# Kernel optimization log

Hardware: AMD Instinct MI355X
Metric: run time of the kernel (lower is better)

The kernel has to match this reference:

```python
import jax, jax.numpy as jnp
import numpy as np

D_MODEL = 512
N_HEADS = 8
D_HEAD = D_MODEL // N_HEADS
SCALE = D_HEAD ** -0.5


def _rel_shift(x):
    # x: (b, h, qlen, klen) -> Transformer-XL relative shift
    b, h, qlen, klen = x.shape
    x = jnp.pad(x, ((0, 0), (0, 0), (0, 0), (1, 0)))        # (b,h,q,k+1)
    x = x.reshape(b, h, klen + 1, qlen)
    x = x[:, :, 1:, :].reshape(b, h, qlen, klen)
    return x


def setup_inputs() -> dict:
    key = jax.random.key(0)
    ks = jax.random.split(key, 12)
    B, S = 2, 2048
    P = 2 * S - 1
    w = lambda k, shape: (jax.random.normal(k, shape, jnp.float32) * 0.02)
    return {
        "x": jax.random.normal(ks[0], (B, S, D_MODEL), jnp.float32),
        "pos_emb": jax.random.normal(ks[1], (P, D_MODEL), jnp.float32),
        "Wq": w(ks[2], (D_MODEL, D_MODEL)), "bq": jnp.zeros((D_MODEL,), jnp.float32),
        "Wk": w(ks[3], (D_MODEL, D_MODEL)), "bk": jnp.zeros((D_MODEL,), jnp.float32),
        "Wv": w(ks[4], (D_MODEL, D_MODEL)), "bv": jnp.zeros((D_MODEL,), jnp.float32),
        "Wp": w(ks[5], (D_MODEL, D_MODEL)),
        "Wo": w(ks[6], (D_MODEL, D_MODEL)), "bo": jnp.zeros((D_MODEL,), jnp.float32),
        "pos_bias_u": w(ks[7], (N_HEADS, D_HEAD)),
        "pos_bias_v": w(ks[8], (N_HEADS, D_HEAD)),
    }


def reference(x, pos_emb, Wq, bq, Wk, bk, Wv, bv, Wp, Wo, bo, pos_bias_u, pos_bias_v):
    B, S, _ = x.shape
    # projections (torch Linear: y = x @ W^T + b; here W stored as (in, out))
    q = (x @ Wq + bq).reshape(B, S, N_HEADS, D_HEAD)
    k = (x @ Wk + bk).reshape(B, S, N_HEADS, D_HEAD)
    v = (x @ Wv + bv).reshape(B, S, N_HEADS, D_HEAD)
    p = (pos_emb @ Wp).reshape(-1, N_HEADS, D_HEAD)  # (2S-1, H, D)

    # content score: (q + u) @ k^T  -> (B,H,S,S)
    content = jnp.einsum("bshd,bthd->bhst", q + pos_bias_u, k)
    # position score: (q + v_bias) @ p^T -> (B,H,S,2S-1), then rel_shift
    pos = jnp.einsum("bshd,phd->bhsp", q + pos_bias_v, p)
    pos = _rel_shift(pos)[..., :S]  # trim to kv_len

    attn = jax.nn.softmax((content + pos) * SCALE, axis=-1)
    out = jnp.einsum("bhst,bthd->bshd", attn, v).reshape(B, S, D_MODEL)
    out = out @ Wo + bo
    return out
```

## Files before the change

kernel.cpp:

```cpp
#include <hip/hip_runtime.h>

#define DM    512
#define NH    8
#define DH    64
#define SEQ   2048
#define PLEN  4095
#define NB    2
#define ATT_SCALE 0.125f

typedef __attribute__((ext_vector_type(8))) _Float16 half8;
typedef __attribute__((ext_vector_type(4))) float   floatx4;

__device__ __forceinline__ void gll16(const _Float16* g, _Float16* l) {
    __builtin_amdgcn_global_load_lds(
        (const __attribute__((address_space(1))) void*)g,
        (__attribute__((address_space(3))) void*)l, 16, 0, 0);
}

__global__ __launch_bounds__(256)
void prep(const float* __restrict__ x, const float* __restrict__ pe,
          const float* __restrict__ W0, const float* __restrict__ W1,
          const float* __restrict__ W2, const float* __restrict__ W3,
          const float* __restrict__ W4,
          _Float16* __restrict__ x16, _Float16* __restrict__ pe16,
          _Float16* __restrict__ Wt)
{
    __shared__ _Float16 tile[64 * 72];
    const int z = blockIdx.z;
    const int t = threadIdx.x;

    if (z < 2) {
        const float* src = z ? pe : x;
        _Float16* dst = z ? pe16 : x16;
        const long n = z ? (long)PLEN * DM : (long)NB * SEQ * DM;
        const long i = ((long)blockIdx.x * 256 + t) * 8;
        if (i >= n) return;
        float4 f0 = *(const float4*)(src + i);
        float4 f1 = *(const float4*)(src + i + 4);
        half8 o;
        o[0] = (_Float16)f0.x; o[1] = (_Float16)f0.y;
        o[2] = (_Float16)f0.z; o[3] = (_Float16)f0.w;
        o[4] = (_Float16)f1.x; o[5] = (_Float16)f1.y;
        o[6] = (_Float16)f1.z; o[7] = (_Float16)f1.w;
        *(half8*)(dst + i) = o;
        return;
    }
    if (blockIdx.x >= 64) return;
    const int wz = z - 2;
    const float* W = (wz == 0) ? W0 : (wz == 1) ? W1 : (wz == 2) ? W2
                   : (wz == 3) ? W3 : W4;
    _Float16* dst_base = Wt + (size_t)wz * DM * DM;
    const int n0 = (blockIdx.x & 7) * 64, k0 = (blockIdx.x >> 3) * 64;
    {
        const int kr = t >> 2, nch = (t & 3) * 16;
        const float* src = W + (size_t)(k0 + kr) * DM + n0 + nch;
        float4 f0 = *(const float4*)(src + 0);
        float4 f1 = *(const float4*)(src + 4);
        float4 f2 = *(const float4*)(src + 8);
        float4 f3 = *(const float4*)(src + 12);
        _Float16* trow = &tile[kr * 72 + nch];
        trow[0]  = (_Float16)f0.x; trow[1]  = (_Float16)f0.y;
        trow[2]  = (_Float16)f0.z; trow[3]  = (_Float16)f0.w;
        trow[4]  = (_Float16)f1.x; trow[5]  = (_Float16)f1.y;
        trow[6]  = (_Float16)f1.z; trow[7]  = (_Float16)f1.w;
        trow[8]  = (_Float16)f2.x; trow[9]  = (_Float16)f2.y;
        trow[10] = (_Float16)f2.z; trow[11] = (_Float16)f2.w;
        trow[12] = (_Float16)f3.x; trow[13] = (_Float16)f3.y;
        trow[14] = (_Float16)f3.z; trow[15] = (_Float16)f3.w;
    }
    __syncthreads();
    {
        const int nr = t >> 2, kch = (t & 3) * 16;
        half8 o0, o1;
#pragma unroll
        for (int i = 0; i < 8; ++i) o0[i] = tile[(kch + i) * 72 + nr];
#pragma unroll
        for (int i = 0; i < 8; ++i) o1[i] = tile[(kch + 8 + i) * 72 + nr];
        _Float16* dst = dst_base + (size_t)(n0 + nr) * DM + k0 + kch;
        *(half8*)dst = o0;
        *(half8*)(dst + 8) = o1;
    }
}

__global__ __launch_bounds__(256)
void gemm_qkvp(const _Float16* __restrict__ X, const _Float16* __restrict__ Pe,
               const _Float16* __restrict__ Wt,
               const float* __restrict__ bq, const float* __restrict__ bk,
               const float* __restrict__ bv, const float* __restrict__ bu,
               const float* __restrict__ bvb,
               _Float16* __restrict__ qu16, _Float16* __restrict__ qv16,
               _Float16* __restrict__ k16, _Float16* __restrict__ vt16,
               _Float16* __restrict__ p16)
{
    __shared__ _Float16 aS[64 * 72];
    __shared__ _Float16 wS[64 * 72];

    const int t = threadIdx.x;
    const int w = t >> 6, lane = t & 63, quad = lane >> 4, l16 = lane & 15;
    const int z = blockIdx.z;
    const int n0 = blockIdx.x * 64;
    const int m0 = blockIdx.y * 64;
    const int srow = t >> 2, sch = (t & 3) * 16;
    const _Float16* A = (z == 3) ? Pe : X;
    const _Float16* Wz = Wt + (size_t)z * DM * DM;

    int arow = m0 + srow;
    if (z == 3 && arow > PLEN - 1) arow = PLEN - 1;
    const _Float16* arowp = A + (size_t)arow * DM + sch;
    const _Float16* wrowp = Wz + (size_t)(n0 + srow) * DM + sch;

    floatx4 acc[4];
#pragma unroll
    for (int ct = 0; ct < 4; ++ct) acc[ct] = (floatx4){0.f, 0.f, 0.f, 0.f};

    half8 pa0 = *(const half8*)arowp;
    half8 pa1 = *(const half8*)(arowp + 8);
    half8 pw0 = *(const half8*)wrowp;
    half8 pw1 = *(const half8*)(wrowp + 8);

    for (int k0 = 0; k0 < DM; k0 += 64) {
        __syncthreads();
        *(half8*)&aS[srow * 72 + sch]     = pa0;
        *(half8*)&aS[srow * 72 + sch + 8] = pa1;
        *(half8*)&wS[srow * 72 + sch]     = pw0;
        *(half8*)&wS[srow * 72 + sch + 8] = pw1;
        __syncthreads();
        if (k0 + 64 < DM) {
            pa0 = *(const half8*)(arowp + k0 + 64);
            pa1 = *(const half8*)(arowp + k0 + 72);
            pw0 = *(const half8*)(wrowp + k0 + 64);
            pw1 = *(const half8*)(wrowp + k0 + 72);
        }
#pragma unroll
        for (int kb = 0; kb < 2; ++kb) {
            half8 af = *(const half8*)&aS[(16 * w + l16) * 72 + kb * 32 + quad * 8];
#pragma unroll
            for (int ct = 0; ct < 4; ++ct) {
                half8 bf = *(const half8*)&wS[(16 * ct + l16) * 72 + kb * 32 + quad * 8];
                acc[ct] = __builtin_amdgcn_mfma_f32_16x16x32_f16(af, bf, acc[ct], 0, 0, 0);
            }
        }
    }

    const int h = n0 >> 6;
    if (z == 0) {
#pragma unroll
        for (int ct = 0; ct < 4; ++ct) {
            const int n = n0 + 16 * ct + l16;
            const float bval = bq[n], uval = bu[n], vval = bvb[n];
#pragma unroll
            for (int r = 0; r < 4; ++r) {
                const int m = m0 + 16 * w + 4 * quad + r;
                const int b = m >> 11, s = m & 2047;
                const size_t dst = ((size_t)((h * NB + b) * SEQ) + s) * DH + (n & 63);
                const float q = acc[ct][r] + bval;
                qu16[dst] = (_Float16)((q + uval) * ATT_SCALE);
                qv16[dst] = (_Float16)((q + vval) * ATT_SCALE);
            }
        }
    } else if (z == 1) {
#pragma unroll
        for (int ct = 0; ct < 4; ++ct) {
            const int n = n0 + 16 * ct + l16;
            const float bval = bk[n];
#pragma unroll
            for (int r = 0; r < 4; ++r) {
                const int m = m0 + 16 * w + 4 * quad + r;
                const int b = m >> 11, s = m & 2047;
                k16[((size_t)((h * NB + b) * SEQ) + s) * DH + (n & 63)] =
                    (_Float16)(acc[ct][r] + bval);
            }
        }
    } else if (z == 2) {
        __syncthreads();
#pragma unroll
        for (int ct = 0; ct < 4; ++ct) {
            const float bval = bv[n0 + 16 * ct + l16];
#pragma unroll
            for (int r = 0; r < 4; ++r)
                aS[(16 * w + 4 * quad + r) * 72 + 16 * ct + l16] =
                    (_Float16)(acc[ct][r] + bval);
        }
        __syncthreads();
        const int b = m0 >> 11, s0 = m0 & 2047;
        const int drow = t >> 2;
        half8 o0, o1;
#pragma unroll
        for (int i = 0; i < 8; ++i) o0[i] = aS[(sch + i) * 72 + drow];
#pragma unroll
        for (int i = 0; i < 8; ++i) o1[i] = aS[(sch + 8 + i) * 72 + drow];
        _Float16* dst = vt16 + ((size_t)((h * NB + b) * DH) + drow) * SEQ + s0 + sch;
        *(half8*)dst = o0;
        *(half8*)(dst + 8) = o1;
    } else {
#pragma unroll
        for (int ct = 0; ct < 4; ++ct) {
            const int n = n0 + 16 * ct + l16;
#pragma unroll
            for (int r = 0; r < 4; ++r) {
                const int m = m0 + 16 * w + 4 * quad + r;
                if (m < PLEN)
                    p16[((size_t)h * PLEN + m) * DH + (n & 63)] = (_Float16)acc[ct][r];
            }
        }
    }
}

__global__ __launch_bounds__(256, 3)
void relattn_mfma(const _Float16* __restrict__ QU,
                  const _Float16* __restrict__ QV,
                  const _Float16* __restrict__ Kp,
                  const _Float16* __restrict__ VT,
                  const _Float16* __restrict__ Pp,
                  float* __restrict__ Opart,
                  float* __restrict__ Lpart)
{
    __shared__ _Float16 kbuf[2 * 4096];
    __shared__ _Float16 vbuf[4096];
    __shared__ _Float16 pring[2 * 4096];
    __shared__ _Float16 tS[64 * 72];

    const int t = threadIdx.x;
    const int w = t >> 6, lane = t & 63, quad = lane >> 4, l16 = lane & 15;
    const int i0 = blockIdx.x * 64;
    const int h = blockIdx.y;
    const int b = blockIdx.z & 1, jh = blockIdx.z >> 1;
    const size_t hb = (size_t)(h * NB + b);
    const int cbase = 48 - 16 * w;
    const int jbeg = jh * (SEQ / 2), jend = jbeg + (SEQ / 2);

    half8 qa[2], va[2];
    {
        const _Float16* qrow = QU + (hb * SEQ + i0 + 16 * w + l16) * DH + quad * 8;
        const _Float16* vrow = QV + (hb * SEQ + i0 + 16 * w + l16) * DH + quad * 8;
        qa[0] = *(const half8*)qrow;       qa[1] = *(const half8*)(qrow + 32);
        va[0] = *(const half8*)vrow;       va[1] = *(const half8*)(vrow + 32);
    }

    floatx4 O[4];
    float lsum[4] = {0.f, 0.f, 0.f, 0.f};
#pragma unroll
    for (int ct = 0; ct < 4; ++ct) O[ct] = (floatx4){0.f, 0.f, 0.f, 0.f};

    const _Float16* Kbase = Kp + hb * SEQ * DH;
    const _Float16* Vbase = VT + hb * DH * SEQ;
    const _Float16* Pbase = Pp + (size_t)h * PLEN * DH;
    const int rbase0 = (SEQ - 1) - i0 - 63;
    const int w0beg  = rbase0 + jbeg;

    const int kx = l16 & 7;
    const int hox0 = ((quad) ^ kx) * 8;
    const int hox1 = ((4 + quad) ^ kx) * 8;

    const int l3 = lane >> 3, pos = lane & 7;

    int prow64[5], pcar[5];
#pragma unroll
    for (int c2 = 0; c2 < 5; ++c2) {
        const int off = cbase + 16 * c2 + l16;
        prow64[c2] = (off & 63) * 64;
        pcar[c2]   = (off >> 6) & 1;
    }

#define STAGE_K(DST, J0)                                                       \
    { _Pragma("unroll") for (int I = 0; I < 2; ++I) {                          \
        const int cid = w * 2 + I;                                             \
        const int row = cid * 8 + l3;                                          \
        gll16(Kbase + (size_t)((J0) + row) * DH + ((pos ^ l3) << 3),           \
              (DST) + cid * 512); } }

#define STAGE_V(J0)                                                            \
    { _Pragma("unroll") for (int I = 0; I < 2; ++I) {                          \
        const int cid = w * 2 + I;                                             \
        const int row = cid * 8 + l3;                                          \
        gll16(Vbase + (size_t)row * SEQ + (J0) + ((pos ^ l3) << 3),            \
              vbuf + cid * 512); } }

#define STAGE_P(RELB)                                                         \
    { _Float16* pdst = pring + ((((RELB) >> 6) & 1) * 4096);                  \
      _Pragma("unroll") for (int I = 0; I < 2; ++I) {                         \
        const int cid = w * 2 + I;                                            \
        int ar = w0beg + (RELB) + cid * 8 + l3;                               \
        if (ar > PLEN - 1) ar = PLEN - 1;                                     \
        gll16(Pbase + (size_t)ar * DH + ((pos ^ l3) << 3),                    \
              pdst + cid * 512); } }

    STAGE_K(kbuf, jbeg);
    STAGE_P(0);
    STAGE_P(64);

    int cur = 0, par = 0;
    for (int j0 = jbeg; j0 < jend; j0 += 64) {
        asm volatile("s_waitcnt vmcnt(0)" ::: "memory");
        __builtin_amdgcn_s_barrier();
        asm volatile("" ::: "memory");

        const _Float16* kS = kbuf + cur * 4096;
        const bool more = (j0 + 64 < jend);

        STAGE_V(j0);
        if (more) STAGE_K(kbuf + (cur ^ 1) * 4096, j0 + 64);

        floatx4 Tacc[5];
#pragma unroll
        for (int c2 = 0; c2 < 5; ++c2) Tacc[c2] = (floatx4){0.f, 0.f, 0.f, 0.f};
#pragma unroll
        for (int c2 = 0; c2 < 5; ++c2) {
            const _Float16* pp = pring + ((pcar[c2] ^ par) * 4096) + prow64[c2];
            half8 bf0 = *(const half8*)(pp + hox0);
            half8 bf1 = *(const half8*)(pp + hox1);
            Tacc[c2] = __builtin_amdgcn_mfma_f32_16x16x32_f16(va[0], bf0, Tacc[c2], 0, 0, 0);
            Tacc[c2] = __builtin_amdgcn_mfma_f32_16x16x32_f16(va[1], bf1, Tacc[c2], 0, 0, 0);
        }

        asm volatile("" ::: "memory");
        __builtin_amdgcn_s_barrier();
        asm volatile("" ::: "memory");
        if (more) STAGE_P((j0 - jbeg) + 128);

        floatx4 Sc[4];
#pragma unroll
        for (int ct = 0; ct < 4; ++ct) Sc[ct] = (floatx4){0.f, 0.f, 0.f, 0.f};
#pragma unroll
        for (int ct = 0; ct < 4; ++ct) {
            half8 bf0 = *(const half8*)&kS[(16 * ct + l16) * 64 + hox0];
            half8 bf1 = *(const half8*)&kS[(16 * ct + l16) * 64 + hox1];
            Sc[ct] = __builtin_amdgcn_mfma_f32_16x16x32_f16(qa[0], bf0, Sc[ct], 0, 0, 0);
            Sc[ct] = __builtin_amdgcn_mfma_f32_16x16x32_f16(qa[1], bf1, Sc[ct], 0, 0, 0);
        }

#pragma unroll
        for (int r = 0; r < 4; ++r) {
            const int u  = l16 - 4 * quad - r + 15;
            const int dl = u & 15;
            const int s  = u >> 4;
            const int pidx = (((quad << 4) | dl) << 2);
            float rot[5];
#pragma unroll
            for (int c2 = 0; c2 < 5; ++c2)
                rot[c2] = __int_as_float(__builtin_amdgcn_ds_bpermute(
                    pidx, __float_as_int(Tacc[c2][r])));
#pragma unroll
            for (int ct = 0; ct < 4; ++ct) {
                const float tv = s ? rot[ct + 1] : rot[ct];
                const float e = __expf(Sc[ct][r] + tv);
                Sc[ct][r] = e;
                lsum[r] += e;
            }
        }

#pragma unroll
        for (int ct = 0; ct < 4; ++ct)
#pragma unroll
            for (int r = 0; r < 4; ++r)
                tS[(16 * w + 4 * quad + r) * 72 + 16 * ct + l16] = (_Float16)Sc[ct][r];
        asm volatile("" ::: "memory");

        if (more) asm volatile("s_waitcnt vmcnt(4)" ::: "memory");
        else      asm volatile("s_waitcnt vmcnt(0)" ::: "memory");
        __builtin_amdgcn_s_barrier();
        asm volatile("" ::: "memory");

#pragma unroll
        for (int kb = 0; kb < 2; ++kb) {
            half8 af = *(const half8*)&tS[(16 * w + l16) * 72 + kb * 32 + quad * 8];
            const int hox = kb ? hox1 : hox0;
#pragma unroll
            for (int ct = 0; ct < 4; ++ct) {
                half8 bf = *(const half8*)&vbuf[(16 * ct + l16) * 64 + hox];
                O[ct] = __builtin_amdgcn_mfma_f32_16x16x32_f16(af, bf, O[ct], 0, 0, 0);
            }
        }
        asm volatile("" ::: "memory");
        cur ^= 1; par ^= 1;
    }
#undef STAGE_K
#undef STAGE_V
#undef STAGE_P

    float* Op = Opart + (size_t)jh * NB * SEQ * DM;
    float* Lp = Lpart + (size_t)jh * NH * NB * SEQ;
#pragma unroll
    for (int r = 0; r < 4; ++r) {
#pragma unroll
        for (int m = 1; m < 16; m <<= 1) lsum[r] += __shfl_xor(lsum[r], m);
        const int row = i0 + 16 * w + 4 * quad + r;
        if (l16 == 0) Lp[hb * SEQ + row] = lsum[r];
        float* orow = Op + (size_t)(b * SEQ + row) * DM + h * DH;
#pragma unroll
        for (int ct = 0; ct < 4; ++ct)
            orow[16 * ct + l16] = O[ct][r];
    }
}

__global__ __launch_bounds__(256)
void attn_combine(const float* __restrict__ O0, const float* __restrict__ O1,
                  const float* __restrict__ L0, const float* __restrict__ L1,
                  _Float16* __restrict__ Out)
{
    const int e = (blockIdx.x * 256 + threadIdx.x) * 8;
    const int m = e >> 9;
    const int col = e & 511;
    const int h = col >> 6;
    const int b = m >> 11, i = m & 2047;
    const int li = (h * NB + b) * SEQ + i;
    const float inv = 1.f / (L0[li] + L1[li]);
    float4 a0 = *(const float4*)(O0 + e);
    float4 a1 = *(const float4*)(O0 + e + 4);
    float4 c0 = *(const float4*)(O1 + e);
    float4 c1 = *(const float4*)(O1 + e + 4);
    half8 o;
    o[0] = (_Float16)((a0.x + c0.x) * inv);
    o[1] = (_Float16)((a0.y + c0.y) * inv);
    o[2] = (_Float16)((a0.z + c0.z) * inv);
    o[3] = (_Float16)((a0.w + c0.w) * inv);
    o[4] = (_Float16)((a1.x + c1.x) * inv);
    o[5] = (_Float16)((a1.y + c1.y) * inv);
    o[6] = (_Float16)((a1.z + c1.z) * inv);
    o[7] = (_Float16)((a1.w + c1.w) * inv);
    *(half8*)(Out + e) = o;
}

__global__ __launch_bounds__(256)
void gemm_out(const _Float16* __restrict__ A, const _Float16* __restrict__ Wt,
              const float* __restrict__ bias, float* __restrict__ Out)
{
    __shared__ _Float16 aS[64 * 72];
    __shared__ _Float16 wS[64 * 72];

    const int t = threadIdx.x;
    const int w = t >> 6, lane = t & 63, quad = lane >> 4, l16 = lane & 15;
    const int n0 = blockIdx.x * 64;
    const int m0 = blockIdx.y * 64;
    const int srow = t >> 2, sch = (t & 3) * 16;

    const _Float16* arowp = A + (size_t)(m0 + srow) * DM + sch;
    const _Float16* wrowp = Wt + (size_t)(n0 + srow) * DM + sch;

    floatx4 acc[4];
#pragma unroll
    for (int ct = 0; ct < 4; ++ct) acc[ct] = (floatx4){0.f, 0.f, 0.f, 0.f};

    half8 pa0 = *(const half8*)arowp;
    half8 pa1 = *(const half8*)(arowp + 8);
    half8 pw0 = *(const half8*)wrowp;
    half8 pw1 = *(const half8*)(wrowp + 8);

    for (int k0 = 0; k0 < DM; k0 += 64) {
        __syncthreads();
        *(half8*)&aS[srow * 72 + sch]     = pa0;
        *(half8*)&aS[srow * 72 + sch + 8] = pa1;
        *(half8*)&wS[srow * 72 + sch]     = pw0;
        *(half8*)&wS[srow * 72 + sch + 8] = pw1;
        __syncthreads();
        if (k0 + 64 < DM) {
            pa0 = *(const half8*)(arowp + k0 + 64);
            pa1 = *(const half8*)(arowp + k0 + 72);
            pw0 = *(const half8*)(wrowp + k0 + 64);
            pw1 = *(const half8*)(wrowp + k0 + 72);
        }
#pragma unroll
        for (int kb = 0; kb < 2; ++kb) {
            half8 af = *(const half8*)&aS[(16 * w + l16) * 72 + kb * 32 + quad * 8];
#pragma unroll
            for (int ct = 0; ct < 4; ++ct) {
                half8 bf = *(const half8*)&wS[(16 * ct + l16) * 72 + kb * 32 + quad * 8];
                acc[ct] = __builtin_amdgcn_mfma_f32_16x16x32_f16(af, bf, acc[ct], 0, 0, 0);
            }
        }
    }

#pragma unroll
    for (int ct = 0; ct < 4; ++ct) {
        const int n = n0 + 16 * ct + l16;
        const float bval = bias[n];
#pragma unroll
        for (int r = 0; r < 4; ++r) {
            const int m = m0 + 16 * w + 4 * quad + r;
            Out[(size_t)m * DM + n] = acc[ct][r] + bval;
        }
    }
}

extern "C" void kernel_launch(void* const* d_in, const int* in_sizes, int n_in,
                              void* d_out, int out_size, void* d_ws, size_t ws_size,
                              hipStream_t stream)
{
    (void)in_sizes; (void)n_in; (void)out_size; (void)ws_size;
    const float* x   = (const float*)d_in[0];
    const float* pe  = (const float*)d_in[1];
    const float* Wq  = (const float*)d_in[2];
    const float* bq  = (const float*)d_in[3];
    const float* Wk  = (const float*)d_in[4];
    const float* bk  = (const float*)d_in[5];
    const float* Wv  = (const float*)d_in[6];
    const float* bv  = (const float*)d_in[7];
    const float* Wp  = (const float*)d_in[8];
    const float* Wo  = (const float*)d_in[9];
    const float* bo  = (const float*)d_in[10];
    const float* pbu = (const float*)d_in[11];
    const float* pbv = (const float*)d_in[12];
    float* out = (float*)d_out;

    const size_t nX  = (size_t)NB * SEQ * DM;
    const size_t nPe = (size_t)PLEN * DM;
    const size_t nW  = (size_t)DM * DM;
    const size_t nH  = (size_t)NH * NB * SEQ * DH;
    const size_t nPh = (size_t)NH * PLEN * DH;
    const size_t nL  = (size_t)NH * NB * SEQ;

    _Float16* x16  = (_Float16*)d_ws;
    _Float16* pe16 = x16 + nX;
    _Float16* wt   = pe16 + nPe;
    _Float16* qu16 = wt + 5 * nW;
    _Float16* qv16 = qu16 + nH;
    _Float16* k16  = qv16 + nH;
    _Float16* vt16 = k16 + nH;
    _Float16* p16  = vt16 + nH;
    _Float16* ow16 = p16 + nPh;
    float*    opart = (float*)(ow16 + nX);
    float*    lpart = opart + 2 * nX;

    dim3 blk(256);
    prep<<<dim3(1024, 1, 7), blk, 0, stream>>>(x, pe, Wq, Wk, Wv, Wp, Wo,
                                               x16, pe16, wt);
    gemm_qkvp<<<dim3(8, 64, 4), blk, 0, stream>>>(x16, pe16, wt,
                                                  bq, bk, bv, pbu, pbv,
                                                  qu16, qv16, k16, vt16, p16);
    relattn_mfma<<<dim3(SEQ / 64, NH, NB * 2), blk, 0, stream>>>(
        qu16, qv16, k16, vt16, p16, opart, lpart);
    attn_combine<<<dim3((unsigned)(nX / (256 * 8))), blk, 0, stream>>>(
        opart, opart + nX, lpart, lpart + nL, ow16);
    gemm_out<<<dim3(8, 64), blk, 0, stream>>>(ow16, wt + 4 * nW, bo, out);
}
```

Baseline: 187.5 us.

## Retile QKVP projection GEMM to 128x128 with async LDS double buffering

```diff
diff --git a/kernel.cpp b/kernel.cpp
--- a/kernel.cpp
+++ b/kernel.cpp
@@ -92,116 +92,149 @@
                _Float16* __restrict__ k16, _Float16* __restrict__ vt16,
                _Float16* __restrict__ p16)
 {
-    __shared__ _Float16 aS[64 * 72];
-    __shared__ _Float16 wS[64 * 72];
+    __shared__ _Float16 smem[32768];
 
     const int t = threadIdx.x;
     const int w = t >> 6, lane = t & 63, quad = lane >> 4, l16 = lane & 15;
+    const int wr = w >> 1, wc = w & 1;
+    const int l3 = lane >> 3, pos = lane & 7;
     const int z = blockIdx.z;
-    const int n0 = blockIdx.x * 64;
-    const int m0 = blockIdx.y * 64;
-    const int srow = t >> 2, sch = (t & 3) * 16;
+    const int n0 = blockIdx.x * 128;
+    const int m0 = blockIdx.y * 128;
+
     const _Float16* A = (z == 3) ? Pe : X;
     const _Float16* Wz = Wt + (size_t)z * DM * DM;
 
-    int arow = m0 + srow;
-    if (z == 3 && arow > PLEN - 1) arow = PLEN - 1;
-    const _Float16* arowp = A + (size_t)arow * DM + sch;
-    const _Float16* wrowp = Wz + (size_t)(n0 + srow) * DM + sch;
-
-    floatx4 acc[4];
-#pragma unroll
-    for (int ct = 0; ct < 4; ++ct) acc[ct] = (floatx4){0.f, 0.f, 0.f, 0.f};
-
-    half8 pa0 = *(const half8*)arowp;
-    half8 pa1 = *(const half8*)(arowp + 8);
-    half8 pw0 = *(const half8*)wrowp;
-    half8 pw1 = *(const half8*)(wrowp + 8);
-
+    const int kx = l16 & 7;
+    const int hox0 = ((quad) ^ kx) * 8;
+    const int hox1 = ((4 + quad) ^ kx) * 8;
+
+    floatx4 acc[4][4];
+#pragma unroll
+    for (int i = 0; i < 4; ++i)
+#pragma unroll
+        for (int j = 0; j < 4; ++j) acc[i][j] = (floatx4){0.f, 0.f, 0.f, 0.f};
+
+#define QSTAGE(CUR, K0)                                                        \
+    { _Float16* aB = smem + (CUR) * 16384;                                     \
+      _Float16* wB = aB + 8192;                                                \
+      _Pragma("unroll") for (int I = 0; I < 4; ++I) {                          \
+        const int gr = I * 32 + w * 8 + l3;                                    \
+        const int ch = pos ^ l3;                                               \
+        int ar = m0 + gr; if (z == 3 && ar > PLEN - 1) ar = PLEN - 1;          \
+        gll16(A + (size_t)ar * DM + (K0) + ch * 8, aB + I * 2048 + w * 512);   \
+        gll16(Wz + (size_t)(n0 + gr) * DM + (K0) + ch * 8,                     \
+              wB + I * 2048 + w * 512); } }
+
+    QSTAGE(0, 0);
+    int cur = 0;
     for (int k0 = 0; k0 < DM; k0 += 64) {
-        __syncthreads();
-        *(half8*)&aS[srow * 72 + sch]     = pa0;
-        *(half8*)&aS[srow * 72 + sch + 8] = pa1;
-        *(half8*)&wS[srow * 72 + sch]     = pw0;
-        *(half8*)&wS[srow * 72 + sch + 8] = pw1;
-        __syncthreads();
-        if (k0 + 64 < DM) {
-            pa0 = *(const half8*)(arowp + k0 + 64);
-            pa1 = *(const half8*)(arowp + k0 + 72);
-            pw0 = *(const half8*)(wrowp + k0 + 64);
-            pw1 = *(const half8*)(wrowp + k0 + 72);
-        }
+        asm volatile("s_waitcnt vmcnt(0)" ::: "memory");
+        __builtin_amdgcn_s_barrier();
+        asm volatile("" ::: "memory");
+        if (k0 + 64 < DM) QSTAGE(cur ^ 1, k0 + 64);
+        const _Float16* aB = smem + cur * 16384;
+        const _Float16* wB = aB + 8192;
 #pragma unroll
         for (int kb = 0; kb < 2; ++kb) {
-            half8 af = *(const half8*)&aS[(16 * w + l16) * 72 + kb * 32 + quad * 8];
-#pragma unroll
-            for (int ct = 0; ct < 4; ++ct) {
-                half8 bf = *(const half8*)&wS[(16 * ct + l16) * 72 + kb * 32 + quad * 8];
-                acc[ct] = __builtin_amdgcn_mfma_f32_16x16x32_f16(af, bf, acc[ct], 0, 0, 0);
-            }
-        }
-    }
-
-    const int h = n0 >> 6;
+            const int hox = kb ? hox1 : hox0;
+            half8 af[4], bf[4];
+#pragma unroll
+            for (int i = 0; i < 4; ++i)
+                af[i] = *(const half8*)&aB[(wr * 64 + i * 16 + l16) * 64 + hox];
+#pragma unroll
+            for (int j = 0; j < 4; ++j)
+                bf[j] = *(const half8*)&wB[(wc * 64 + j * 16 + l16) * 64 + hox];
+#pragma unroll
+            for (int i = 0; i < 4; ++i)
+#pragma unroll
+                for (int j = 0; j < 4; ++j)
+                    acc[i][j] = __builtin_amdgcn_mfma_f32_16x16x32_f16(
+                        af[i], bf[j], acc[i][j], 0, 0, 0);
+        }
+        cur ^= 1;
+    }
+#undef QSTAGE
+
+    const int hh = (n0 >> 6) + wc;
+    const int bb = m0 >> 11;
+    const int sbase = (m0 & 2047) + wr * 64;
+
     if (z == 0) {
 #pragma unroll
-        for (int ct = 0; ct < 4; ++ct) {
-            const int n = n0 + 16 * ct + l16;
+        for (int j = 0; j < 4; ++j) {
+            const int n = n0 + wc * 64 + j * 16 + l16;
+            const int d = j * 16 + l16 - (wc ? 64 : 0) + (wc ? 64 : 0);
             const float bval = bq[n], uval = bu[n], vval = bvb[n];
 #pragma unroll
-            for (int r = 0; r < 4; ++r) {
-                const int m = m0 + 16 * w + 4 * quad + r;
-                const int b = m >> 11, s = m & 2047;
-                const size_t dst = ((size_t)((h * NB + b) * SEQ) + s) * DH + (n & 63);
-                const float q = acc[ct][r] + bval;
-                qu16[dst] = (_Float16)((q + uval) * ATT_SCALE);
-                qv16[dst] = (_Float16)((q + vval) * ATT_SCALE);
-            }
+            for (int i = 0; i < 4; ++i)
+#pragma unroll
+                for (int r = 0; r < 4; ++r) {
+                    const int s = sbase + i * 16 + 4 * quad + r;
+                    const size_t dst = ((size_t)((hh * NB + bb) * SEQ) + s) * DH + (n & 63);
+                    const float q = acc[i][j][r] + bval;
+                    qu16[dst] = (_Float16)((q + uval) * ATT_SCALE);
+                    qv16[dst] = (_Float16)((q + vval) * ATT_SCALE);
+                }
+            (void)d;
         }
     } else if (z == 1) {
 #pragma unroll
-        for (int ct = 0; ct < 4; ++ct) {
-            const int n = n0 + 16 * ct + l16;
+        for (int j = 0; j < 4; ++j) {
+            const int n = n0 + wc * 64 + j * 16 + l16;
             const float bval = bk[n];
 #pragma unroll
-            for (int r = 0; r < 4; ++r) {
-                const int m = m0 + 16 * w + 4 * quad + r;
-                const int b = m >> 11, s = m & 2047;
-                k16[((size_t)((h * NB + b) * SEQ) + s) * DH + (n & 63)] =
-                    (_Float16)(acc[ct][r] + bval);
-            }
+            for (int i = 0; i < 4; ++i)
+#pragma unroll
+                for (int r = 0; r < 4; ++r) {
+                    const int s = sbase + i * 16 + 4 * quad + r;
+                    k16[((size_t)((hh * NB + bb) * SEQ) + s) * DH + (n & 63)] =
+                        (_Float16)(acc[i][j][r] + bval);
+                }
         }
     } else if (z == 2) {
         __syncthreads();
-#pragma unroll
-        for (int ct = 0; ct < 4; ++ct) {
-            const float bval = bv[n0 + 16 * ct + l16];
-#pragma unroll
-            for (int r = 0; r < 4; ++r)
-                aS[(16 * w + 4 * quad + r) * 72 + 16 * ct + l16] =
-                    (_Float16)(acc[ct][r] + bval);
+        _Float16* tr = smem;
+#pragma unroll
+        for (int j = 0; j < 4; ++j) {
+            const int ncol = wc * 64 + j * 16 + l16;
+            const float bval = bv[n0 + ncol];
+#pragma unroll
+            for (int i = 0; i < 4; ++i)
+#pragma unroll
+                for (int r = 0; r < 4; ++r)
+                    tr[(wr * 64 + i * 16 + 4 * quad + r) * 132 + ncol] =
+                        (_Float16)(acc[i][j][r] + bval);
         }
         __syncthreads();
-        const int b = m0 >> 11, s0 = m0 & 2047;
-        const int drow = t >> 2;
-        half8 o0, o1;
-#pragma unroll
-        for (int i = 0; i < 8; ++i) o0[i] = aS[(sch + i) * 72 + drow];
-#pragma unroll
-        for (int i = 0; i < 8; ++i) o1[i] = aS[(sch + 8 + i) * 72 + drow];
-        _Float16* dst = vt16 + ((size_t)((h * NB + b) * DH) + drow) * SEQ + s0 + sch;
-        *(half8*)dst = o0;
-        *(half8*)(dst + 8) = o1;
+        {
+            const int col = t >> 1;
+            const int half = t & 1;
+            const int h2 = (n0 + col) >> 6, d = (n0 + col) & 63;
+            const int s0 = (m0 & 2047) + half * 64;
+            _Float16* dst = vt16 + ((size_t)((h2 * NB + bb) * DH) + d) * SEQ + s0;
+#pragma unroll
+            for (int c = 0; c < 8; ++c) {
+                half8 o;
+#pragma unroll
+                for (int k = 0; k < 8; ++k)
+                    o[k] = tr[(half * 64 + c * 8 + k) * 132 + col];
+                *(half8*)(dst + c * 8) = o;
+            }
+        }
     } else {
 #pragma unroll
-        for (int ct = 0; ct < 4; ++ct) {
-            const int n = n0 + 16 * ct + l16;
-#pragma unroll
-            for (int r = 0; r < 4; ++r) {
-                const int m = m0 + 16 * w + 4 * quad + r;
-                if (m < PLEN)
-                    p16[((size_t)h * PLEN + m) * DH + (n & 63)] = (_Float16)acc[ct][r];
-            }
+        for (int j = 0; j < 4; ++j) {
+            const int n = n0 + wc * 64 + j * 16 + l16;
+#pragma unroll
+            for (int i = 0; i < 4; ++i)
+#pragma unroll
+                for (int r = 0; r < 4; ++r) {
+                    const int m = m0 + wr * 64 + i * 16 + 4 * quad + r;
+                    if (m < PLEN)
+                        p16[((size_t)hh * PLEN + m) * DH + (n & 63)] =
+                            (_Float16)acc[i][j][r];
+                }
         }
     }
 }
@@ -524,7 +557,7 @@
     dim3 blk(256);
     prep<<<dim3(1024, 1, 7), blk, 0, stream>>>(x, pe, Wq, Wk, Wv, Wp, Wo,
                                                x16, pe16, wt);
-    gemm_qkvp<<<dim3(8, 64, 4), blk, 0, stream>>>(x16, pe16, wt,
+    gemm_qkvp<<<dim3(4, 32, 4), blk, 0, stream>>>(x16, pe16, wt,
                                                   bq, bk, bv, pbu, pbv,
                                                   qu16, qv16, k16, vt16, p16);
     relattn_mfma<<<dim3(SEQ / 64, NH, NB * 2), blk, 0, stream>>>(
```

Measured after the change: 178.3 us. 1.05x faster.
